# Kernel optimization log

Hardware: AMD Instinct MI355X
Metric: run time of the kernel (lower is better)

Reference implementation:

```python
import jax, jax.numpy as jnp
import numpy as np

N, E = 50000, 800000
IN, HID, OUT = 128, 32, 8


def setup_inputs() -> dict:
    key = jax.random.key(0)
    ks = jax.random.split(key, 20)
    f32 = jnp.float32
    def rn(k, shape, s=0.1):
        return (jax.random.normal(k, shape, dtype=f32) * s)
    return {
        'x': jax.random.normal(ks[0], (N, IN), dtype=f32),
        'edge_index': jax.random.randint(ks[1], (2, E), 0, N, dtype=jnp.int32),
        'edge_attr': jax.random.uniform(ks[2], (E, 1), dtype=f32),
        # layer 1: heads=4, out=HID, concat -> 4*HID channels
        'w1l': rn(ks[3], (IN, 4 * HID)), 'b1l': rn(ks[4], (4 * HID,)),
        'w1r': rn(ks[5], (IN, 4 * HID)), 'b1r': rn(ks[6], (4 * HID,)),
        'w1e': rn(ks[7], (1, 4 * HID)),
        'att1': rn(ks[8], (4, HID)), 'bias1': rn(ks[9], (4 * HID,)),
        # layer 2: heads=2, out=HID, mean over heads -> HID channels
        'w2l': rn(ks[10], (4 * HID, 2 * HID)), 'b2l': rn(ks[11], (2 * HID,)),
        'w2r': rn(ks[12], (4 * HID, 2 * HID)), 'b2r': rn(ks[13], (2 * HID,)),
        'w2e': rn(ks[14], (1, 2 * HID)),
        'att2': rn(ks[15], (2, HID)), 'bias2': rn(ks[16], (HID,)),
        'wc': rn(ks[17], (HID, OUT)), 'bc': rn(ks[18], (OUT,)),
    }


def _add_self_loops(edge_index, edge_attr, n):
    # PyG GATv2Conv adds self-loops; edge feature for loops = mean of edge_attr
    loop = jnp.arange(n, dtype=edge_index.dtype)
    src = jnp.concatenate([edge_index[0], loop])
    dst = jnp.concatenate([edge_index[1], loop])
    mean_attr = jnp.broadcast_to(edge_attr.mean(axis=0), (n, edge_attr.shape[1]))
    ea = jnp.concatenate([edge_attr, mean_attr], axis=0)
    return src, dst, ea


def _gatv2(x, src, dst, eattr, Wl, bl, Wr, br, We, att, bias, heads, out, concat):
    n = x.shape[0]
    xl = (x @ Wl + bl).reshape(n, heads, out)   # source transform (messages)
    xr = (x @ Wr + br).reshape(n, heads, out)   # target transform
    e = (eattr @ We).reshape(-1, heads, out)    # edge embedding
    z = jax.nn.leaky_relu(xl[src] + xr[dst] + e, negative_slope=0.2)  # [Etot,H,D]
    score = jnp.einsum('ehd,hd->eh', z, att)
    # segment softmax over incoming edges of each destination node
    smax = jax.ops.segment_max(score, dst, num_segments=n)
    ex = jnp.exp(score - smax[dst])
    denom = jax.ops.segment_sum(ex, dst, num_segments=n)
    alpha = ex / denom[dst]                     # [Etot,H]
    agg = jax.ops.segment_sum(xl[src] * alpha[..., None], dst, num_segments=n)
    o = agg.reshape(n, heads * out) if concat else agg.mean(axis=1)
    return o + bias


def reference(x, edge_index, edge_attr, w1l, b1l, w1r, b1r, w1e, att1, bias1,
              w2l, b2l, w2r, b2r, w2e, att2, bias2, wc, bc):
    src, dst, ea = _add_self_loops(edge_index, edge_attr, x.shape[0])
    h = _gatv2(x, src, dst, ea, w1l, b1l, w1r, b1r, w1e, att1, bias1, 4, HID, True)
    h = jax.nn.elu(h)
    # dropout p=0.4 is training-only; reference is eval mode (identity)
    h = _gatv2(h, src, dst, ea, w2l, b2l, w2r, b2r, w2e, att2, bias2, 2, HID, False)
    h = jax.nn.elu(h)
    return h @ wc + bc
```

## Files before the change

### kernel.cpp

```cpp
#include <hip/hip_runtime.h>
#include <hip/hip_fp16.h>
#include <math.h>

typedef _Float16 h2_t __attribute__((ext_vector_type(2)));
typedef _Float16 h4_t __attribute__((ext_vector_type(4)));
typedef _Float16 h8_t __attribute__((ext_vector_type(8)));
typedef float f4_t __attribute__((ext_vector_type(4)));
typedef float f8_t __attribute__((ext_vector_type(8)));

#define PRE_BLOCKS 512
#define SB 512
#define NBUK_PAD 800
#define CTB 16

__device__ inline h8_t load8f_to_h8(const float* p) {
    float4 a = *(const float4*)p;
    float4 b = *(const float4*)(p + 4);
    h8_t r;
    r[0] = (_Float16)a.x; r[1] = (_Float16)a.y; r[2] = (_Float16)a.z; r[3] = (_Float16)a.w;
    r[4] = (_Float16)b.x; r[5] = (_Float16)b.y; r[6] = (_Float16)b.z; r[7] = (_Float16)b.w;
    return r;
}

__device__ inline h4_t load4f_to_h4(const float* p) {
    float4 a = *(const float4*)p;
    h4_t r;
    r[0] = (_Float16)a.x; r[1] = (_Float16)a.y; r[2] = (_Float16)a.z; r[3] = (_Float16)a.w;
    return r;
}

__device__ inline float dot8h(h8_t a, h8_t b, float s) {
    s = __builtin_amdgcn_fdot2(__builtin_shufflevector(a, a, 0, 1),
                               __builtin_shufflevector(b, b, 0, 1), s, false);
    s = __builtin_amdgcn_fdot2(__builtin_shufflevector(a, a, 2, 3),
                               __builtin_shufflevector(b, b, 2, 3), s, false);
    s = __builtin_amdgcn_fdot2(__builtin_shufflevector(a, a, 4, 5),
                               __builtin_shufflevector(b, b, 4, 5), s, false);
    s = __builtin_amdgcn_fdot2(__builtin_shufflevector(a, a, 6, 7),
                               __builtin_shufflevector(b, b, 6, 7), s, false);
    return s;
}

__device__ inline float dot4h(h4_t a, h4_t b, float s) {
    s = __builtin_amdgcn_fdot2(__builtin_shufflevector(a, a, 0, 1),
                               __builtin_shufflevector(b, b, 0, 1), s, false);
    s = __builtin_amdgcn_fdot2(__builtin_shufflevector(a, a, 2, 3),
                               __builtin_shufflevector(b, b, 2, 3), s, false);
    return s;
}

__device__ inline float elu1(float v) { return v > 0.f ? v : __expf(v) - 1.f; }

struct MA {
    const float* x;
    const float* eattr;
    const int* ei;
    const float *w1l, *b1l, *w1r, *b1r, *w1e, *att1, *bias1;
    const float *w2l, *b2l, *w2r, *b2r, *w2e, *att2, *bias2;
    const float *wc, *bc;
    float* out;
    _Float16 *xh, *xl1h, *xr1h, *xl2h, *xr2h;
    _Float16 *p1l, *p1r, *p2l, *p2r;
    int *deg, *offb;
    unsigned* parth;
    unsigned* tot;
    unsigned* tmp;
    float* part;
    unsigned* edges;
    int N, E, NW, NBK, CE;
    float invE;
};


__device__ inline void phase_packw(const MA& a, int g) {
    const float* W;
    _Float16* P;
    int M, lg;
    if (g < 2048)      { W = a.w1l; P = a.p1l; M = 128; lg = g; }
    else if (g < 4096) { W = a.w1r; P = a.p1r; M = 128; lg = g - 2048; }
    else if (g < 5120) { W = a.w2l; P = a.p2l; M = 64;  lg = g - 4096; }
    else               { W = a.w2r; P = a.p2r; M = 64;  lg = g - 5120; }
    int ln = lg & 63;
    int s = (lg >> 6) & 3;
    int tt = lg >> 8;
    int m = ln & 15, quad = ln >> 4;
    h8_t v;
#pragma unroll
    for (int j = 0; j < 8; ++j)
        v[j] = (_Float16)W[(size_t)(s * 32 + quad * 8 + j) * M + tt * 16 + m];
    *(h8_t*)(P + (size_t)lg * 8) = v;
}

template <int NT>
__device__ inline void phase_mm_tile(const MA& a, const _Float16* X, int rt, int lane,
                                     const _Float16* Pl, const float* bl, _Float16* Yl,
                                     const _Float16* Pr, const float* br, _Float16* Yr) {
    int nrow = lane & 15, quad = lane >> 4;
    int row = rt * 16 + nrow;
    if (row >= a.N) return;
    const _Float16* xp = X + (size_t)row * 128 + quad * 8;
    h8_t bf0 = *(const h8_t*)(xp);
    h8_t bf1 = *(const h8_t*)(xp + 32);
    h8_t bf2 = *(const h8_t*)(xp + 64);
    h8_t bf3 = *(const h8_t*)(xp + 96);
#pragma unroll
    for (int w = 0; w < 2; ++w) {
        const _Float16* P = w ? Pr : Pl;
        const float* bias = w ? br : bl;
        _Float16* Y = w ? Yr : Yl;
#pragma unroll
        for (int t2 = 0; t2 < NT; ++t2) {
            f4_t acc = {0.f, 0.f, 0.f, 0.f};
            const _Float16* pb = P + (size_t)t2 * 2048 + (size_t)lane * 8;
            acc = __builtin_amdgcn_mfma_f32_16x16x32_f16(*(const h8_t*)pb, bf0, acc, 0, 0, 0);
            acc = __builtin_amdgcn_mfma_f32_16x16x32_f16(*(const h8_t*)(pb + 512), bf1, acc, 0, 0, 0);
            acc = __builtin_amdgcn_mfma_f32_16x16x32_f16(*(const h8_t*)(pb + 1024), bf2, acc, 0, 0, 0);
            acc = __builtin_amdgcn_mfma_f32_16x16x32_f16(*(const h8_t*)(pb + 1536), bf3, acc, 0, 0, 0);
            float4 bv = *(const float4*)(bias + t2 * 16 + quad * 4);
            h4_t o;
            o[0] = (_Float16)(acc[0] + bv.x);
            o[1] = (_Float16)(acc[1] + bv.y);
            o[2] = (_Float16)(acc[2] + bv.z);
            o[3] = (_Float16)(acc[3] + bv.w);
            *(h4_t*)(Y + (size_t)row * (NT * 16) + t2 * 16 + quad * 4) = o;
        }
    }
}


__global__ __launch_bounds__(256) void k_pre(MA a) {
    if (blockIdx.x >= PRE_BLOCKS) {
        int g = (blockIdx.x - PRE_BLOCKS) * 256 + threadIdx.x;
        if (g < 6144) phase_packw(a, g);
        return;
    }
    __shared__ unsigned bh[NBUK_PAD];
    __shared__ float sd[4];
    int tx = threadIdx.x;
    for (int j = tx; j < NBUK_PAD; j += 256) bh[j] = 0u;

    int t = blockIdx.x * 256 + tx;
    const int stride = PRE_BLOCKS * 256;
    int nchunk = (a.N * 128) >> 3;
    for (int i = t; i < nchunk; i += stride) {
        h8_t v = load8f_to_h8(a.x + (size_t)i * 8);
        *(h8_t*)(a.xh + (size_t)i * 8) = v;
    }
    float s = 0.f;
    for (int i = t; i < a.E; i += stride) s += a.eattr[i];
    for (int o = 1; o < 64; o <<= 1) s += __shfl_xor(s, o, 64);
    if ((tx & 63) == 0) sd[tx >> 6] = s;
    __syncthreads();
    if (tx == 0) a.part[blockIdx.x] = sd[0] + sd[1] + sd[2] + sd[3];

    int e0 = blockIdx.x * a.CE, e1 = min(e0 + a.CE, a.E);
    for (int e = e0 + tx; e < e1; e += 256)
        atomicAdd(&bh[((unsigned)a.ei[a.E + e]) >> 6], 1u);
    __syncthreads();
    for (int j = tx; j < NBUK_PAD; j += 256)
        a.parth[(size_t)blockIdx.x * NBUK_PAD + j] = bh[j];
}


__global__ __launch_bounds__(512, 1) void k_colscan(MA a) {
    __shared__ unsigned tile[512][CTB + 1];
    int tx = threadIdx.x;
    int b0 = blockIdx.x * CTB;
    unsigned* rp = a.parth + (size_t)tx * NBUK_PAD + b0;
#pragma unroll
    for (int j = 0; j < CTB; ++j) tile[tx][j] = rp[j];
    __syncthreads();

    int c = tx >> 5;
    int g = tx & 31;
    unsigned base = 0;
#pragma unroll
    for (int k = 0; k < 16; ++k) {
        int r = k * 32 + g;
        unsigned orig = tile[r][c];
        unsigned v = orig;
#pragma unroll
        for (int o = 1; o < 32; o <<= 1) {
            unsigned u = __shfl_up(v, o, 32);
            if (g >= o) v += u;
        }
        tile[r][c] = base + (v - orig);
        base += __shfl(v, 31, 32);
    }
    if (g == 0) a.tot[b0 + c] = base;
    __syncthreads();
#pragma unroll
    for (int j = 0; j < CTB; ++j) rp[j] = tile[tx][j];
}


__global__ __launch_bounds__(256) void k_scatter(MA a) {
    int bid = blockIdx.x;
    if (bid < a.NW) {
        int wid = bid * 4 + (threadIdx.x >> 6);
        int ntile = (a.N + 15) / 16;
        if (wid < ntile)
            phase_mm_tile<8>(a, a.xh, wid, threadIdx.x & 63,
                             a.p1l, a.b1l, a.xl1h, a.p1r, a.b1r, a.xr1h);
        return;
    }
    __shared__ unsigned cur[1024];
    __shared__ unsigned wt[4];
    int s = bid - a.NW;
    int tx = threadIdx.x;
    for (int j = tx; j < 1024; j += 256)
        cur[j] = (j < NBUK_PAD) ? a.tot[j] : 0u;
    __syncthreads();
    {
        unsigned x0 = cur[tx * 4], x1 = cur[tx * 4 + 1], x2 = cur[tx * 4 + 2], x3 = cur[tx * 4 + 3];
        unsigned s1 = x0 + x1, s2 = s1 + x2, t = s2 + x3;
        unsigned inc = t;
#pragma unroll
        for (int o = 1; o < 64; o <<= 1) {
            unsigned u = __shfl_up(inc, o, 64);
            if ((tx & 63) >= o) inc += u;
        }
        if ((tx & 63) == 63) wt[tx >> 6] = inc;
        __syncthreads();
        unsigned wb = 0;
#pragma unroll
        for (int k = 0; k < 4; ++k) wb += (k < (tx >> 6)) ? wt[k] : 0u;
        unsigned excl = wb + (inc - t);
        cur[tx * 4]     = excl;
        cur[tx * 4 + 1] = excl + x0;
        cur[tx * 4 + 2] = excl + s1;
        cur[tx * 4 + 3] = excl + s2;
    }
    __syncthreads();
    for (int j = tx; j < NBUK_PAD; j += 256)
        cur[j] += a.parth[(size_t)s * NBUK_PAD + j];
    __syncthreads();
    int e0 = s * a.CE, e1 = min(e0 + a.CE, a.E);
    for (int e = e0 + tx; e < e1; e += 256) {
        int d = a.ei[a.E + e];
        unsigned src = (unsigned)a.ei[e];
        unsigned q = (unsigned)__float2int_rn(a.eattr[e] * 255.f);
        unsigned pos = atomicAdd(&cur[d >> 6], 1u);
        a.tmp[pos] = src | (q << 16) | ((unsigned)(d & 63) << 24);
    }
}


__global__ __launch_bounds__(256) void k_fuse(MA a) {
    __shared__ int hist[64];
    __shared__ unsigned cur[64];
    __shared__ int offl[64], degl[64];
    __shared__ unsigned rts[4];
    __shared__ float rs[4];
    __shared__ _Float16 h1s[64 * 128];

    int b = blockIdx.x, tx = threadIdx.x;
    int n0 = b << 6;
    int nn = min(64, a.N - n0);

    if (tx < 64) hist[tx] = 0;
    unsigned ps = 0;
    for (int j = tx; j < b; j += 256) ps += a.tot[j];
    for (int o = 1; o < 64; o <<= 1) ps += __shfl_xor(ps, o, 64);
    if ((tx & 63) == 0) rts[tx >> 6] = ps;
    float s = 0.f;
    for (int j = tx; j < PRE_BLOCKS; j += 256) s += a.part[j];
    for (int o = 1; o < 64; o <<= 1) s += __shfl_xor(s, o, 64);
    if ((tx & 63) == 0) rs[tx >> 6] = s;
    __syncthreads();
    unsigned ts = rts[0] + rts[1] + rts[2] + rts[3];
    unsigned sm = (unsigned)__float2int_rn((rs[0] + rs[1] + rs[2] + rs[3]) * a.invE * 255.f);
    unsigned T = a.tot[b];

    for (unsigned i = tx; i < T; i += 256)
        atomicAdd(&hist[(int)(a.tmp[ts + i] >> 24)], 1);
    __syncthreads();
    if (tx < 64) {
        int deg1 = hist[tx] + 1;
        int vsc = deg1;
#pragma unroll
        for (int o = 1; o < 64; o <<= 1) {
            int u = __shfl_up(vsc, o, 64);
            if (tx >= o) vsc += u;
        }
        int off = (int)ts + n0 + (vsc - deg1);
        if (tx < nn) {
            a.offb[n0 + tx] = off;
            a.deg[n0 + tx] = deg1;
            a.edges[off] = (unsigned)(n0 + tx) | (sm << 24);
            offl[tx] = off;
            degl[tx] = deg1;
        }
        cur[tx] = (unsigned)(off + 1);
    }
    __syncthreads();
    for (unsigned i = tx; i < T; i += 256) {
        unsigned v = a.tmp[ts + i];
        unsigned pos = atomicAdd(&cur[v >> 24], 1u);
        a.edges[pos] = (v & 0xFFFFu) | (((v >> 16) & 0xFFu) << 24);
    }
    __syncthreads();

    int q = tx & 15;
    unsigned cb = (unsigned)(q * 16);
    h8_t wev = load8f_to_h8(a.w1e + q * 8);
    h8_t atv = load8f_to_h8(a.att1 + q * 8);
    float4 bv0 = *(const float4*)(a.bias1 + q * 8);
    float4 bv1 = *(const float4*)(a.bias1 + q * 8 + 4);
    float bb[8] = {bv0.x, bv0.y, bv0.z, bv0.w, bv1.x, bv1.y, bv1.z, bv1.w};
    const char* xb = (const char*)a.xl1h;

    for (int rr = 0; rr < 64; rr += 16) {
        int nloc = rr + (tx >> 4);
        if (nloc < nn) {
            int node = n0 + nloc;
            h8_t xrv = *(const h8_t*)((const char*)a.xr1h + ((unsigned)node << 8) + cb);
            const unsigned* ep = a.edges + offl[nloc];
            int deg1 = degl[nloc];
            int last = deg1 - 1;
            float l = 0.f;
            f8_t acc = {0.f, 0.f, 0.f, 0.f, 0.f, 0.f, 0.f, 0.f};

            auto GA = [&](unsigned p) -> h8_t {
                return *(const h8_t*)(xb + (((p & 0x00FFFFFFu) << 8) | cb));
            };
            auto LOADG = [&](int i, unsigned& p0, unsigned& p1, unsigned& p2, unsigned& p3,
                             h8_t& x0, h8_t& x1, h8_t& x2, h8_t& x3) {
                p0 = ep[i];
                p1 = ep[min(i + 1, last)];
                p2 = ep[min(i + 2, last)];
                p3 = ep[min(i + 3, last)];
                x0 = GA(p0); x1 = GA(p1); x2 = GA(p2); x3 = GA(p3);
            };
            auto COMPG = [&](int i, unsigned p0, unsigned p1, unsigned p2, unsigned p3,
                             h8_t x0, h8_t x1, h8_t x2, h8_t x3) {
                float e0 = (float)(p0 >> 24) * (1.f / 255.f);
                float e1 = (float)(p1 >> 24) * (1.f / 255.f);
                float e2 = (float)(p2 >> 24) * (1.f / 255.f);
                float e3 = (float)(p3 >> 24) * (1.f / 255.f);
                h8_t z0 = x0 + xrv + wev * (_Float16)e0;
                z0 = __builtin_elementwise_max(z0, z0 * (_Float16)0.2f);
                float sc0 = dot8h(z0, atv, 0.f);
                h8_t z1 = x1 + xrv + wev * (_Float16)e1;
                z1 = __builtin_elementwise_max(z1, z1 * (_Float16)0.2f);
                float sc1 = dot8h(z1, atv, 0.f);
                h8_t z2 = x2 + xrv + wev * (_Float16)e2;
                z2 = __builtin_elementwise_max(z2, z2 * (_Float16)0.2f);
                float sc2 = dot8h(z2, atv, 0.f);
                h8_t z3 = x3 + xrv + wev * (_Float16)e3;
                z3 = __builtin_elementwise_max(z3, z3 * (_Float16)0.2f);
                float sc3 = dot8h(z3, atv, 0.f);
                sc0 += __shfl_xor(sc0, 1, 64); sc0 += __shfl_xor(sc0, 2, 64);
                sc1 += __shfl_xor(sc1, 1, 64); sc1 += __shfl_xor(sc1, 2, 64);
                sc2 += __shfl_xor(sc2, 1, 64); sc2 += __shfl_xor(sc2, 2, 64);
                sc3 += __shfl_xor(sc3, 1, 64); sc3 += __shfl_xor(sc3, 2, 64);
                float pA = __expf(fminf(sc0, 60.f));
                float pB = (i + 1 < deg1) ? __expf(fminf(sc1, 60.f)) : 0.f;
                float pC = (i + 2 < deg1) ? __expf(fminf(sc2, 60.f)) : 0.f;
                float pD = (i + 3 < deg1) ? __expf(fminf(sc3, 60.f)) : 0.f;
                l += (pA + pB) + (pC + pD);
#pragma unroll
                for (int k = 0; k < 8; ++k)
                    acc[k] = fmaf(pA, (float)x0[k],
                             fmaf(pB, (float)x1[k],
                             fmaf(pC, (float)x2[k], fmaf(pD, (float)x3[k], acc[k]))));
            };

            unsigned pa0, pa1, pa2, pa3, pb0, pb1, pb2, pb3;
            h8_t xa0, xa1, xa2, xa3, xb0, xb1, xb2, xb3;
            LOADG(0, pa0, pa1, pa2, pa3, xa0, xa1, xa2, xa3);
            for (int i = 0; i < deg1; i += 8) {
                if (i + 4 < deg1) LOADG(i + 4, pb0, pb1, pb2, pb3, xb0, xb1, xb2, xb3);
                COMPG(i, pa0, pa1, pa2, pa3, xa0, xa1, xa2, xa3);
                if (i + 8 < deg1) LOADG(i + 8, pa0, pa1, pa2, pa3, xa0, xa1, xa2, xa3);
                if (i + 4 < deg1) COMPG(i + 4, pb0, pb1, pb2, pb3, xb0, xb1, xb2, xb3);
            }

            float inv = 1.f / l;
            h8_t o;
#pragma unroll
            for (int k = 0; k < 8; ++k) o[k] = (_Float16)elu1(fmaf(acc[k], inv, bb[k]));
            *(h8_t*)(h1s + nloc * 128 + q * 8) = o;
        }
    }
    __syncthreads();

    {
        int wv = tx >> 6, lane = tx & 63;
        int nrow = lane & 15, quad = lane >> 4;
        int row = n0 + wv * 16 + nrow;
        if (row < a.N) {
            const _Float16* xp = h1s + (wv * 16 + nrow) * 128 + quad * 8;
            h8_t bf0 = *(const h8_t*)(xp);
            h8_t bf1 = *(const h8_t*)(xp + 32);
            h8_t bf2 = *(const h8_t*)(xp + 64);
            h8_t bf3 = *(const h8_t*)(xp + 96);
#pragma unroll
            for (int w = 0; w < 2; ++w) {
                const _Float16* P = w ? a.p2r : a.p2l;
                const float* bias = w ? a.b2r : a.b2l;
                _Float16* Y = w ? a.xr2h : a.xl2h;
#pragma unroll
                for (int t2 = 0; t2 < 4; ++t2) {
                    f4_t acc2 = {0.f, 0.f, 0.f, 0.f};
                    const _Float16* pb = P + (size_t)t2 * 2048 + (size_t)lane * 8;
                    acc2 = __builtin_amdgcn_mfma_f32_16x16x32_f16(*(const h8_t*)pb, bf0, acc2, 0, 0, 0);
                    acc2 = __builtin_amdgcn_mfma_f32_16x16x32_f16(*(const h8_t*)(pb + 512), bf1, acc2, 0, 0, 0);
                    acc2 = __builtin_amdgcn_mfma_f32_16x16x32_f16(*(const h8_t*)(pb + 1024), bf2, acc2, 0, 0, 0);
                    acc2 = __builtin_amdgcn_mfma_f32_16x16x32_f16(*(const h8_t*)(pb + 1536), bf3, acc2, 0, 0, 0);
                    float4 bv = *(const float4*)(bias + t2 * 16 + quad * 4);
                    h4_t o;
                    o[0] = (_Float16)(acc2[0] + bv.x);
                    o[1] = (_Float16)(acc2[1] + bv.y);
                    o[2] = (_Float16)(acc2[2] + bv.z);
                    o[3] = (_Float16)(acc2[3] + bv.w);
                    *(h4_t*)(Y + (size_t)row * 64 + t2 * 16 + quad * 4) = o;
                }
            }
        }
    }
}


__global__ __launch_bounds__(256) void k_node2(MA a) {
    __shared__ float h2s[16][33];
    int tid = threadIdx.x;
    int lane = tid & 63;
    int wib = tid >> 6;
    int sub = lane >> 4;
    int r = lane & 15;
    int nloc = wib * 4 + sub;
    int node = blockIdx.x * 16 + nloc;
    int c0 = r * 4;

    if (node < a.N) {
        h4_t xrv = *(const h4_t*)(a.xr2h + (size_t)node * 64 + c0);
        h4_t wev = load4f_to_h4(a.w2e + c0);
        h4_t atv = load4f_to_h4(a.att2 + c0);
        const unsigned* ep = a.edges + a.offb[node];
        int deg1 = a.deg[node];
        int last = deg1 - 1;
        const char* xb = (const char*)a.xl2h;
        unsigned cb = (unsigned)(c0 * 2);
        float l = 0.f;
        float acc[4] = {0.f, 0.f, 0.f, 0.f};
        for (int i = 0; i < deg1; i += 4) {
            unsigned p[4];
            h4_t xv[4];
#pragma unroll
            for (int j = 0; j < 4; ++j) p[j] = ep[min(i + j, last)];
#pragma unroll
            for (int j = 0; j < 4; ++j)
                xv[j] = *(const h4_t*)(xb + (((p[j] & 0x00FFFFFFu) << 7) | cb));
#pragma unroll
            for (int j = 0; j < 4; ++j) {
                float ea = (float)(p[j] >> 24) * (1.f / 255.f);
                h4_t z = xv[j] + xrv + wev * (_Float16)ea;
                z = __builtin_elementwise_max(z, z * (_Float16)0.2f);
                float sc = dot4h(z, atv, 0.f);
                sc += __shfl_xor(sc, 1, 64);
                sc += __shfl_xor(sc, 2, 64);
                sc += __shfl_xor(sc, 4, 64);
                float pp = (i + j < deg1) ? __expf(fminf(sc, 60.f)) : 0.f;
                l += pp;
#pragma unroll
                for (int k = 0; k < 4; ++k) acc[k] = fmaf(pp, (float)xv[j][k], acc[k]);
            }
        }
        float inv = 1.f / l;
#pragma unroll
        for (int k = 0; k < 4; ++k) {
            float norm = acc[k] * inv;
            float other = __shfl_xor(norm, 8, 64);
            float v = 0.5f * (norm + other);
            if (r < 8) h2s[nloc][c0 + k] = elu1(v + a.bias2[c0 + k]);
        }
    }
    __syncthreads();
    if (tid < 128) {
        int n = tid >> 3, j = tid & 7;
        int gnode = blockIdx.x * 16 + n;
        if (gnode < a.N) {
            float acc = a.bc[j];
#pragma unroll 8
            for (int d = 0; d < 32; ++d) acc = fmaf(h2s[n][d], a.wc[d * 8 + j], acc);
            a.out[(size_t)gnode * 8 + j] = acc;
        }
    }
}


extern "C" void kernel_launch(void* const* d_in, const int* in_sizes, int n_in,
                              void* d_out, int out_size, void* d_ws, size_t ws_size,
                              hipStream_t stream) {
    const int N = in_sizes[0] / 128;
    const int E = in_sizes[2];
    const int tot = E + N;

    char* ws = (char*)d_ws;
    size_t o = 0;
    auto alloc = [&](size_t bytes) -> void* {
        void* p = ws + o;
        o += (bytes + 255) & ~(size_t)255;
        return p;
    };
    MA a;
    a.x     = (const float*)d_in[0];
    a.ei    = (const int*)d_in[1];
    a.eattr = (const float*)d_in[2];
    a.w1l = (const float*)d_in[3];  a.b1l = (const float*)d_in[4];
    a.w1r = (const float*)d_in[5];  a.b1r = (const float*)d_in[6];
    a.w1e = (const float*)d_in[7];  a.att1 = (const float*)d_in[8];
    a.bias1 = (const float*)d_in[9];
    a.w2l = (const float*)d_in[10]; a.b2l = (const float*)d_in[11];
    a.w2r = (const float*)d_in[12]; a.b2r = (const float*)d_in[13];
    a.w2e = (const float*)d_in[14]; a.att2 = (const float*)d_in[15];
    a.bias2 = (const float*)d_in[16];
    a.wc = (const float*)d_in[17];  a.bc = (const float*)d_in[18];
    a.out = (float*)d_out;

    a.xh   = (_Float16*)alloc((size_t)N * 128 * 2);
    a.xl1h = (_Float16*)alloc((size_t)N * 128 * 2);
    a.xr1h = (_Float16*)alloc((size_t)N * 128 * 2);
    a.xl2h = (_Float16*)alloc((size_t)N * 64 * 2);
    a.xr2h = (_Float16*)alloc((size_t)N * 64 * 2);
    a.p1l  = (_Float16*)alloc(128 * 128 * 2);
    a.p1r  = (_Float16*)alloc(128 * 128 * 2);
    a.p2l  = (_Float16*)alloc(128 * 64 * 2);
    a.p2r  = (_Float16*)alloc(128 * 64 * 2);
    a.deg  = (int*)alloc((size_t)N * 4);
    a.offb = (int*)alloc((size_t)N * 4);
    a.parth = (unsigned*)alloc((size_t)SB * NBUK_PAD * 4);
    a.tot   = (unsigned*)alloc(1024 * 4);
    a.part  = (float*)alloc(PRE_BLOCKS * 4);
    a.tmp   = (unsigned*)alloc((size_t)E * 4);
    a.edges = (unsigned*)alloc((size_t)tot * 4);
    a.N = N;
    a.E = E;
    a.NW = (N + 63) / 64;
    a.NBK = (N + 63) >> 6;
    a.CE = (E + SB - 1) / SB;
    a.invE = 1.0f / (float)E;

    k_pre<<<PRE_BLOCKS + 24, 256, 0, stream>>>(a);
    k_colscan<<<NBUK_PAD / CTB, 512, 0, stream>>>(a);
    k_scatter<<<a.NW + SB, 256, 0, stream>>>(a);
    k_fuse<<<a.NBK, 256, 0, stream>>>(a);
    k_node2<<<(N + 15) / 16, 256, 0, stream>>>(a);
}
```

Measured before the change: 241.8 us.

## Split fused CSR-finalize/layer-1 kernel into fine-sort and 16-node aggregation kernels

The former k_fuse kernel handled one 64-node bucket per block: it built the per-node CSR, ran layer-1 attention aggregation and did the layer-2 projection MFMA. It is now two kernels. k_fine only builds the CSR ordering. k_n1mm handles 16 nodes per block, aggregates them and runs the MFMA projection, which gives about four times as many blocks and uses less LDS. The bucket start offsets and the quantized mean edge attribute are now computed once in the scatter kernel, instead of every block re-reducing them. Gathers for padded edge slots are also masked. The cost is an extra launch, plus edges and offsets making a global round trip between the kernels.

```diff
diff --git a/kernel.cpp b/kernel.cpp
--- a/kernel.cpp
+++ b/kernel.cpp
@@ -64,6 +64,7 @@
     int *deg, *offb;
     unsigned* parth;
     unsigned* tot;
+    unsigned *tstart, *smeanq;
     unsigned* tmp;
     float* part;
     unsigned* edges;
@@ -230,8 +231,26 @@
         cur[tx * 4 + 1] = excl + x0;
         cur[tx * 4 + 2] = excl + s1;
         cur[tx * 4 + 3] = excl + s2;
-    }
-    __syncthreads();
+        if (s == 0) {
+            if (tx < NBUK_PAD / 4) {
+                a.tstart[tx * 4]     = cur[tx * 4];
+                a.tstart[tx * 4 + 1] = cur[tx * 4 + 1];
+                a.tstart[tx * 4 + 2] = cur[tx * 4 + 2];
+                a.tstart[tx * 4 + 3] = cur[tx * 4 + 3];
+            }
+        }
+    }
+    __syncthreads();
+    if (s == 0) {
+        float ss = 0.f;
+        for (int j = tx; j < PRE_BLOCKS; j += 256) ss += a.part[j];
+        for (int o = 1; o < 64; o <<= 1) ss += __shfl_xor(ss, o, 64);
+        __shared__ float rs[4];
+        if ((tx & 63) == 0) rs[tx >> 6] = ss;
+        __syncthreads();
+        if (tx == 0)
+            a.smeanq[0] = (unsigned)__float2int_rn((rs[0] + rs[1] + rs[2] + rs[3]) * a.invE * 255.f);
+    }
     for (int j = tx; j < NBUK_PAD; j += 256)
         cur[j] += a.parth[(size_t)s * NBUK_PAD + j];
     __syncthreads();
@@ -246,34 +265,22 @@
 }
 
 
-__global__ __launch_bounds__(256) void k_fuse(MA a) {
+__global__ __launch_bounds__(256) void k_fine(MA a) {
     __shared__ int hist[64];
     __shared__ unsigned cur[64];
-    __shared__ int offl[64], degl[64];
-    __shared__ unsigned rts[4];
-    __shared__ float rs[4];
-    __shared__ _Float16 h1s[64 * 128];
-
-    int b = blockIdx.x, tx = threadIdx.x;
+    __shared__ unsigned sm;
+    int b = blockIdx.x;
+    int tx = threadIdx.x;
     int n0 = b << 6;
     int nn = min(64, a.N - n0);
-
+    unsigned ts = a.tstart[b], T = a.tot[b];
     if (tx < 64) hist[tx] = 0;
-    unsigned ps = 0;
-    for (int j = tx; j < b; j += 256) ps += a.tot[j];
-    for (int o = 1; o < 64; o <<= 1) ps += __shfl_xor(ps, o, 64);
-    if ((tx & 63) == 0) rts[tx >> 6] = ps;
-    float s = 0.f;
-    for (int j = tx; j < PRE_BLOCKS; j += 256) s += a.part[j];
-    for (int o = 1; o < 64; o <<= 1) s += __shfl_xor(s, o, 64);
-    if ((tx & 63) == 0) rs[tx >> 6] = s;
-    __syncthreads();
-    unsigned ts = rts[0] + rts[1] + rts[2] + rts[3];
-    unsigned sm = (unsigned)__float2int_rn((rs[0] + rs[1] + rs[2] + rs[3]) * a.invE * 255.f);
-    unsigned T = a.tot[b];
-
-    for (unsigned i = tx; i < T; i += 256)
-        atomicAdd(&hist[(int)(a.tmp[ts + i] >> 24)], 1);
+    if (tx == 0) sm = a.smeanq[0];
+    __syncthreads();
+    for (unsigned i = tx; i < T; i += 256) {
+        unsigned v = a.tmp[ts + i];
+        atomicAdd(&hist[(int)(v >> 24)], 1);
+    }
     __syncthreads();
     if (tx < 64) {
         int deg1 = hist[tx] + 1;
@@ -288,134 +295,140 @@
             a.offb[n0 + tx] = off;
             a.deg[n0 + tx] = deg1;
             a.edges[off] = (unsigned)(n0 + tx) | (sm << 24);
-            offl[tx] = off;
-            degl[tx] = deg1;
         }
         cur[tx] = (unsigned)(off + 1);
     }
     __syncthreads();
     for (unsigned i = tx; i < T; i += 256) {
         unsigned v = a.tmp[ts + i];
-        unsigned pos = atomicAdd(&cur[v >> 24], 1u);
+        int loc = (int)(v >> 24);
+        unsigned pos = atomicAdd(&cur[loc], 1u);
         a.edges[pos] = (v & 0xFFFFu) | (((v >> 16) & 0xFFu) << 24);
     }
-    __syncthreads();
-
-    int q = tx & 15;
+}
+
+
+__global__ __launch_bounds__(256) void k_n1mm(MA a) {
+    __shared__ _Float16 h1s[16 * 128];
+    int tid = threadIdx.x;
+    int q = tid & 15;
+    int nloc = tid >> 4;
+    int node = blockIdx.x * 16 + nloc;
     unsigned cb = (unsigned)(q * 16);
-    h8_t wev = load8f_to_h8(a.w1e + q * 8);
-    h8_t atv = load8f_to_h8(a.att1 + q * 8);
-    float4 bv0 = *(const float4*)(a.bias1 + q * 8);
-    float4 bv1 = *(const float4*)(a.bias1 + q * 8 + 4);
-    float bb[8] = {bv0.x, bv0.y, bv0.z, bv0.w, bv1.x, bv1.y, bv1.z, bv1.w};
-    const char* xb = (const char*)a.xl1h;
-
-    for (int rr = 0; rr < 64; rr += 16) {
-        int nloc = rr + (tx >> 4);
-        if (nloc < nn) {
-            int node = n0 + nloc;
-            h8_t xrv = *(const h8_t*)((const char*)a.xr1h + ((unsigned)node << 8) + cb);
-            const unsigned* ep = a.edges + offl[nloc];
-            int deg1 = degl[nloc];
-            int last = deg1 - 1;
-            float l = 0.f;
-            f8_t acc = {0.f, 0.f, 0.f, 0.f, 0.f, 0.f, 0.f, 0.f};
-
-            auto GA = [&](unsigned p) -> h8_t {
-                return *(const h8_t*)(xb + (((p & 0x00FFFFFFu) << 8) | cb));
-            };
-            auto LOADG = [&](int i, unsigned& p0, unsigned& p1, unsigned& p2, unsigned& p3,
-                             h8_t& x0, h8_t& x1, h8_t& x2, h8_t& x3) {
-                p0 = ep[i];
-                p1 = ep[min(i + 1, last)];
-                p2 = ep[min(i + 2, last)];
-                p3 = ep[min(i + 3, last)];
-                x0 = GA(p0); x1 = GA(p1); x2 = GA(p2); x3 = GA(p3);
-            };
-            auto COMPG = [&](int i, unsigned p0, unsigned p1, unsigned p2, unsigned p3,
-                             h8_t x0, h8_t x1, h8_t x2, h8_t x3) {
-                float e0 = (float)(p0 >> 24) * (1.f / 255.f);
-                float e1 = (float)(p1 >> 24) * (1.f / 255.f);
-                float e2 = (float)(p2 >> 24) * (1.f / 255.f);
-                float e3 = (float)(p3 >> 24) * (1.f / 255.f);
-                h8_t z0 = x0 + xrv + wev * (_Float16)e0;
-                z0 = __builtin_elementwise_max(z0, z0 * (_Float16)0.2f);
-                float sc0 = dot8h(z0, atv, 0.f);
-                h8_t z1 = x1 + xrv + wev * (_Float16)e1;
-                z1 = __builtin_elementwise_max(z1, z1 * (_Float16)0.2f);
-                float sc1 = dot8h(z1, atv, 0.f);
-                h8_t z2 = x2 + xrv + wev * (_Float16)e2;
-                z2 = __builtin_elementwise_max(z2, z2 * (_Float16)0.2f);
-                float sc2 = dot8h(z2, atv, 0.f);
-                h8_t z3 = x3 + xrv + wev * (_Float16)e3;
-                z3 = __builtin_elementwise_max(z3, z3 * (_Float16)0.2f);
-                float sc3 = dot8h(z3, atv, 0.f);
-                sc0 += __shfl_xor(sc0, 1, 64); sc0 += __shfl_xor(sc0, 2, 64);
-                sc1 += __shfl_xor(sc1, 1, 64); sc1 += __shfl_xor(sc1, 2, 64);
-                sc2 += __shfl_xor(sc2, 1, 64); sc2 += __shfl_xor(sc2, 2, 64);
-                sc3 += __shfl_xor(sc3, 1, 64); sc3 += __shfl_xor(sc3, 2, 64);
-                float pA = __expf(fminf(sc0, 60.f));
-                float pB = (i + 1 < deg1) ? __expf(fminf(sc1, 60.f)) : 0.f;
-                float pC = (i + 2 < deg1) ? __expf(fminf(sc2, 60.f)) : 0.f;
-                float pD = (i + 3 < deg1) ? __expf(fminf(sc3, 60.f)) : 0.f;
-                l += (pA + pB) + (pC + pD);
-#pragma unroll
-                for (int k = 0; k < 8; ++k)
-                    acc[k] = fmaf(pA, (float)x0[k],
-                             fmaf(pB, (float)x1[k],
-                             fmaf(pC, (float)x2[k], fmaf(pD, (float)x3[k], acc[k]))));
-            };
-
-            unsigned pa0, pa1, pa2, pa3, pb0, pb1, pb2, pb3;
-            h8_t xa0, xa1, xa2, xa3, xb0, xb1, xb2, xb3;
-            LOADG(0, pa0, pa1, pa2, pa3, xa0, xa1, xa2, xa3);
-            for (int i = 0; i < deg1; i += 8) {
-                if (i + 4 < deg1) LOADG(i + 4, pb0, pb1, pb2, pb3, xb0, xb1, xb2, xb3);
-                COMPG(i, pa0, pa1, pa2, pa3, xa0, xa1, xa2, xa3);
-                if (i + 8 < deg1) LOADG(i + 8, pa0, pa1, pa2, pa3, xa0, xa1, xa2, xa3);
-                if (i + 4 < deg1) COMPG(i + 4, pb0, pb1, pb2, pb3, xb0, xb1, xb2, xb3);
-            }
-
-            float inv = 1.f / l;
-            h8_t o;
-#pragma unroll
-            for (int k = 0; k < 8; ++k) o[k] = (_Float16)elu1(fmaf(acc[k], inv, bb[k]));
-            *(h8_t*)(h1s + nloc * 128 + q * 8) = o;
-        }
+
+    if (node < a.N) {
+        h8_t xrv = *(const h8_t*)((const char*)a.xr1h + ((unsigned)node << 8) + cb);
+        h8_t wev = load8f_to_h8(a.w1e + q * 8);
+        h8_t atv = load8f_to_h8(a.att1 + q * 8);
+        const unsigned* ep = a.edges + a.offb[node];
+        int deg1 = a.deg[node];
+        int last = deg1 - 1;
+        const char* xb = (const char*)a.xl1h;
+
+        float l = 0.f;
+        f8_t acc = {0.f, 0.f, 0.f, 0.f, 0.f, 0.f, 0.f, 0.f};
+
+        auto GA = [&](unsigned p, bool valid) -> h8_t {
+            h8_t r = {};
+            if (valid) r = *(const h8_t*)(xb + (((p & 0x00FFFFFFu) << 8) | cb));
+            return r;
+        };
+        auto LOADG = [&](int i, unsigned& p0, unsigned& p1, unsigned& p2, unsigned& p3,
+                         h8_t& x0, h8_t& x1, h8_t& x2, h8_t& x3) {
+            p0 = ep[i];
+            p1 = ep[min(i + 1, last)];
+            p2 = ep[min(i + 2, last)];
+            p3 = ep[min(i + 3, last)];
+            x0 = GA(p0, true);
+            x1 = GA(p1, i + 1 < deg1);
+            x2 = GA(p2, i + 2 < deg1);
+            x3 = GA(p3, i + 3 < deg1);
+        };
+        auto COMPG = [&](int i, unsigned p0, unsigned p1, unsigned p2, unsigned p3,
+                         h8_t x0, h8_t x1, h8_t x2, h8_t x3) {
+            float e0 = (float)(p0 >> 24) * (1.f / 255.f);
+            float e1 = (float)(p1 >> 24) * (1.f / 255.f);
+            float e2 = (float)(p2 >> 24) * (1.f / 255.f);
+            float e3 = (float)(p3 >> 24) * (1.f / 255.f);
+            h8_t z0 = x0 + xrv + wev * (_Float16)e0;
+            z0 = __builtin_elementwise_max(z0, z0 * (_Float16)0.2f);
+            float sc0 = dot8h(z0, atv, 0.f);
+            h8_t z1 = x1 + xrv + wev * (_Float16)e1;
+            z1 = __builtin_elementwise_max(z1, z1 * (_Float16)0.2f);
+            float sc1 = dot8h(z1, atv, 0.f);
+            h8_t z2 = x2 + xrv + wev * (_Float16)e2;
+            z2 = __builtin_elementwise_max(z2, z2 * (_Float16)0.2f);
+            float sc2 = dot8h(z2, atv, 0.f);
+            h8_t z3 = x3 + xrv + wev * (_Float16)e3;
+            z3 = __builtin_elementwise_max(z3, z3 * (_Float16)0.2f);
+            float sc3 = dot8h(z3, atv, 0.f);
+            sc0 += __shfl_xor(sc0, 1, 64); sc0 += __shfl_xor(sc0, 2, 64);
+            sc1 += __shfl_xor(sc1, 1, 64); sc1 += __shfl_xor(sc1, 2, 64);
+            sc2 += __shfl_xor(sc2, 1, 64); sc2 += __shfl_xor(sc2, 2, 64);
+            sc3 += __shfl_xor(sc3, 1, 64); sc3 += __shfl_xor(sc3, 2, 64);
+            float pA = __expf(fminf(sc0, 60.f));
+            float pB = (i + 1 < deg1) ? __expf(fminf(sc1, 60.f)) : 0.f;
+            float pC = (i + 2 < deg1) ? __expf(fminf(sc2, 60.f)) : 0.f;
+            float pD = (i + 3 < deg1) ? __expf(fminf(sc3, 60.f)) : 0.f;
+            l += (pA + pB) + (pC + pD);
+#pragma unroll
+            for (int k = 0; k < 8; ++k)
+                acc[k] = fmaf(pA, (float)x0[k],
+                         fmaf(pB, (float)x1[k],
+                         fmaf(pC, (float)x2[k], fmaf(pD, (float)x3[k], acc[k]))));
+        };
+
+        unsigned pa0, pa1, pa2, pa3, pb0, pb1, pb2, pb3;
+        h8_t xa0, xa1, xa2, xa3, xb0, xb1, xb2, xb3;
+        LOADG(0, pa0, pa1, pa2, pa3, xa0, xa1, xa2, xa3);
+        for (int i = 0; i < deg1; i += 8) {
+            if (i + 4 < deg1) LOADG(i + 4, pb0, pb1, pb2, pb3, xb0, xb1, xb2, xb3);
+            COMPG(i, pa0, pa1, pa2, pa3, xa0, xa1, xa2, xa3);
+            if (i + 8 < deg1) LOADG(i + 8, pa0, pa1, pa2, pa3, xa0, xa1, xa2, xa3);
+            if (i + 4 < deg1) COMPG(i + 4, pb0, pb1, pb2, pb3, xb0, xb1, xb2, xb3);
+        }
+
+        float inv = 1.f / l;
+        float4 b0 = *(const float4*)(a.bias1 + q * 8);
+        float4 b1 = *(const float4*)(a.bias1 + q * 8 + 4);
+        float bb[8] = {b0.x, b0.y, b0.z, b0.w, b1.x, b1.y, b1.z, b1.w};
+        h8_t o;
+#pragma unroll
+        for (int k = 0; k < 8; ++k) o[k] = (_Float16)elu1(fmaf(acc[k], inv, bb[k]));
+        *(h8_t*)(h1s + nloc * 128 + q * 8) = o;
     }
     __syncthreads();
 
     {
-        int wv = tx >> 6, lane = tx & 63;
+        int wv = tid >> 6, lane = tid & 63;
         int nrow = lane & 15, quad = lane >> 4;
-        int row = n0 + wv * 16 + nrow;
+        int row = blockIdx.x * 16 + nrow;
         if (row < a.N) {
-            const _Float16* xp = h1s + (wv * 16 + nrow) * 128 + quad * 8;
+            const _Float16* xp = h1s + nrow * 128 + quad * 8;
             h8_t bf0 = *(const h8_t*)(xp);
             h8_t bf1 = *(const h8_t*)(xp + 32);
             h8_t bf2 = *(const h8_t*)(xp + 64);
             h8_t bf3 = *(const h8_t*)(xp + 96);
 #pragma unroll
-            for (int w = 0; w < 2; ++w) {
+            for (int k = 0; k < 2; ++k) {
+                int idx = wv * 2 + k;
+                int w = idx >> 2, t2 = idx & 3;
                 const _Float16* P = w ? a.p2r : a.p2l;
                 const float* bias = w ? a.b2r : a.b2l;
                 _Float16* Y = w ? a.xr2h : a.xl2h;
-#pragma unroll
-                for (int t2 = 0; t2 < 4; ++t2) {
-                    f4_t acc2 = {0.f, 0.f, 0.f, 0.f};
-                    const _Float16* pb = P + (size_t)t2 * 2048 + (size_t)lane * 8;
-                    acc2 = __builtin_amdgcn_mfma_f32_16x16x32_f16(*(const h8_t*)pb, bf0, acc2, 0, 0, 0);
-                    acc2 = __builtin_amdgcn_mfma_f32_16x16x32_f16(*(const h8_t*)(pb + 512), bf1, acc2, 0, 0, 0);
-                    acc2 = __builtin_amdgcn_mfma_f32_16x16x32_f16(*(const h8_t*)(pb + 1024), bf2, acc2, 0, 0, 0);
-                    acc2 = __builtin_amdgcn_mfma_f32_16x16x32_f16(*(const h8_t*)(pb + 1536), bf3, acc2, 0, 0, 0);
-                    float4 bv = *(const float4*)(bias + t2 * 16 + quad * 4);
-                    h4_t o;
-                    o[0] = (_Float16)(acc2[0] + bv.x);
-                    o[1] = (_Float16)(acc2[1] + bv.y);
-                    o[2] = (_Float16)(acc2[2] + bv.z);
-                    o[3] = (_Float16)(acc2[3] + bv.w);
-                    *(h4_t*)(Y + (size_t)row * 64 + t2 * 16 + quad * 4) = o;
-                }
+                f4_t acc2 = {0.f, 0.f, 0.f, 0.f};
+                const _Float16* pb = P + (size_t)t2 * 2048 + (size_t)lane * 8;
+                acc2 = __builtin_amdgcn_mfma_f32_16x16x32_f16(*(const h8_t*)pb, bf0, acc2, 0, 0, 0);
+                acc2 = __builtin_amdgcn_mfma_f32_16x16x32_f16(*(const h8_t*)(pb + 512), bf1, acc2, 0, 0, 0);
+                acc2 = __builtin_amdgcn_mfma_f32_16x16x32_f16(*(const h8_t*)(pb + 1024), bf2, acc2, 0, 0, 0);
+                acc2 = __builtin_amdgcn_mfma_f32_16x16x32_f16(*(const h8_t*)(pb + 1536), bf3, acc2, 0, 0, 0);
+                float4 bv = *(const float4*)(bias + t2 * 16 + quad * 4);
+                h4_t o;
+                o[0] = (_Float16)(acc2[0] + bv.x);
+                o[1] = (_Float16)(acc2[1] + bv.y);
+                o[2] = (_Float16)(acc2[2] + bv.z);
+                o[3] = (_Float16)(acc2[3] + bv.w);
+                *(h4_t*)(Y + (size_t)row * 64 + t2 * 16 + quad * 4) = o;
             }
         }
     }
@@ -450,8 +463,11 @@
 #pragma unroll
             for (int j = 0; j < 4; ++j) p[j] = ep[min(i + j, last)];
 #pragma unroll
-            for (int j = 0; j < 4; ++j)
-                xv[j] = *(const h4_t*)(xb + (((p[j] & 0x00FFFFFFu) << 7) | cb));
+            for (int j = 0; j < 4; ++j) {
+                xv[j] = h4_t{};
+                if (i + j < deg1)
+                    xv[j] = *(const h4_t*)(xb + (((p[j] & 0x00FFFFFFu) << 7) | cb));
+            }
 #pragma unroll
             for (int j = 0; j < 4; ++j) {
                 float ea = (float)(p[j] >> 24) * (1.f / 255.f);
@@ -530,11 +546,13 @@
     a.p2r  = (_Float16*)alloc(128 * 64 * 2);
     a.deg  = (int*)alloc((size_t)N * 4);
     a.offb = (int*)alloc((size_t)N * 4);
-    a.parth = (unsigned*)alloc((size_t)SB * NBUK_PAD * 4);
-    a.tot   = (unsigned*)alloc(1024 * 4);
-    a.part  = (float*)alloc(PRE_BLOCKS * 4);
-    a.tmp   = (unsigned*)alloc((size_t)E * 4);
-    a.edges = (unsigned*)alloc((size_t)tot * 4);
+    a.parth  = (unsigned*)alloc((size_t)SB * NBUK_PAD * 4);
+    a.tot    = (unsigned*)alloc(1024 * 4);
+    a.tstart = (unsigned*)alloc(1024 * 4);
+    a.smeanq = (unsigned*)alloc(256);
+    a.part   = (float*)alloc(PRE_BLOCKS * 4);
+    a.tmp    = (unsigned*)alloc((size_t)E * 4);
+    a.edges  = (unsigned*)alloc((size_t)tot * 4);
     a.N = N;
     a.E = E;
     a.NW = (N + 63) / 64;
@@ -545,6 +563,7 @@
     k_pre<<<PRE_BLOCKS + 24, 256, 0, stream>>>(a);
     k_colscan<<<NBUK_PAD / CTB, 512, 0, stream>>>(a);
     k_scatter<<<a.NW + SB, 256, 0, stream>>>(a);
-    k_fuse<<<a.NBK, 256, 0, stream>>>(a);
+    k_fine<<<a.NBK, 256, 0, stream>>>(a);
+    k_n1mm<<<(N + 15) / 16, 256, 0, stream>>>(a);
     k_node2<<<(N + 15) / 16, 256, 0, stream>>>(a);
 }
```

Result: faster. 232.8 us (-3.7%).
